# Optimization experiments

Measured on AMD Instinct MI355X. Metric: run time of the kernel, lower is better.

## Reference

```python
import jax, jax.numpy as jnp
import numpy as np

KSIZE, STRIDE, SCALE = 7, 4, 10.0


def _same_pad_amounts(n, k, s):
    out = -(-n // s)
    pad = max(0, (out - 1) * s + k - n)
    return pad // 2, pad - pad // 2, out


def _conv(x, w, b, stride=1, pad=0):
    y = jax.lax.conv_general_dilated(
        x, w, (stride, stride), [(pad, pad), (pad, pad)],
        dimension_numbers=("NCHW", "OIHW", "NCHW"))
    return y + b[None, :, None, None]


def setup_inputs() -> dict:
    key = jax.random.key(0)
    ks = jax.random.split(key, 10)
    B, Cin, H, W = 2, 64, 256, 256
    Ci = 16                       # inter_channels
    d_in = KSIZE * KSIZE * Ci     # 784 = ksize^2 * inter_channels
    d_out = d_in // 4             # 196
    s = 0.02
    return {
        "b": jax.random.normal(ks[0], (B, Cin, H, W), jnp.float32),
        "g_w": jax.random.normal(ks[1], (Ci, Cin, 3, 3), jnp.float32) * s,
        "g_b": jnp.zeros((Ci,), jnp.float32),
        "theta_w": jax.random.normal(ks[2], (Ci, Cin, 1, 1), jnp.float32) * s,
        "theta_b": jnp.zeros((Ci,), jnp.float32),
        "W_w": jax.random.normal(ks[3], (Cin, Ci, 1, 1), jnp.float32) * s,
        "W_b": jnp.zeros((Cin,), jnp.float32),
        "fc1_w": jax.random.normal(ks[4], (d_out, d_in), jnp.float32) * s,
        "fc1_b": jnp.zeros((d_out,), jnp.float32),
        "fc2_w": jax.random.normal(ks[5], (d_out, d_in), jnp.float32) * s,
        "fc2_b": jnp.zeros((d_out,), jnp.float32),
        "thr_w": jax.random.normal(ks[6], (1, Cin, KSIZE, KSIZE), jnp.float32) * s,
        "thr_b": jnp.zeros((1,), jnp.float32),
        "bias_w": jax.random.normal(ks[7], (1, Cin, KSIZE, KSIZE), jnp.float32) * s,
        "bias_b": jnp.zeros((1,), jnp.float32),
    }


def _forward(b, g_w, g_b, theta_w, theta_b, W_w, W_b, fc1_w, fc1_b,
             fc2_w, fc2_b, thr_w, thr_b, bias_w, bias_b):
    B, Cin, H, W = b.shape
    k, s = KSIZE, STRIDE
    pt, pb, Lh = _same_pad_amounts(H, k, s)
    pl, pr, Lw = _same_pad_amounts(W, k, s)
    L = Lh * Lw
    Ci = g_w.shape[0]

    b1 = _conv(b, g_w, g_b, 1, 1)            # [B,Ci,H,W]
    b2 = _conv(b, theta_w, theta_b, 1, 0)    # [B,Ci,H,W]
    b4 = jnp.pad(b, ((0, 0), (0, 0), (pt, pb), (pl, pr)))
    thr = _conv(b4, thr_w, thr_b, s, 0).reshape(B, L)   # per-patch threshold
    bias = _conv(b4, bias_w, bias_b, s, 0).reshape(B, L)  # per-patch bias

    # patch gather indices on the 'same'-padded grid (torch.Unfold order)
    R = (jnp.arange(Lh) * s)[:, None] + jnp.arange(k)[None, :]   # [Lh,k]
    Cc = (jnp.arange(Lw) * s)[:, None] + jnp.arange(k)[None, :]  # [Lw,k]
    Ri = R[:, None, :, None]                                     # -> [Lh,Lw,k,k]
    Cj = Cc[None, :, None, :]

    def patches(x):  # [B,Ci,H,W] -> [B,L,Ci*k*k], flatten order (C,kh,kw)
        xp = jnp.pad(x, ((0, 0), (0, 0), (pt, pb), (pl, pr)))
        p = xp[:, :, Ri, Cj]                       # [B,Ci,Lh,Lw,k,k]
        return p.transpose(0, 2, 3, 1, 4, 5).reshape(B, L, -1)

    wi = patches(b1)     # stride_1 patches of b1
    xi = wi              # b3 = b1 and stride_1 == stride_2 -> identical patches
    pi = patches(b2)     # stride_2 patches of b2, values to aggregate

    wi_f = jax.nn.relu(jnp.einsum("bld,od->blo", wi, fc1_w) + fc1_b)
    xi_f = jax.nn.relu(jnp.einsum("bld,od->blo", xi, fc2_w) + fc2_b)
    score = jnp.einsum("blo,bmo->blm", wi_f, xi_f)   # [B,L,L] patch similarity

    # threshold-gated sparse attention with learned per-patch thr/bias
    mask = (score >= thr[:, :, None]).astype(score.dtype)
    gated = score * mask + bias[:, :, None]
    attn = jax.nn.softmax(gated * SCALE, axis=-1) * mask
    attn = attn / (attn.sum(-1, keepdims=True) + 1e-8)

    agg = jnp.einsum("blm,bmd->bld", attn, pi)       # [B,L,Ci*k*k]
    p6 = agg.reshape(B, Lh, Lw, Ci, k, k).transpose(0, 3, 1, 2, 4, 5)

    # fold back (sum overlaps), normalize by overlap count, crop padding
    Hp, Wp = H + pt + pb, W + pl + pr
    folded = jnp.zeros((B, Ci, Hp, Wp), score.dtype).at[:, :, Ri, Cj].add(p6)
    cnt = jnp.zeros((Hp, Wp), score.dtype).at[Ri, Cj].add(1.0)
    zi = (folded / cnt)[:, :, pl:pl + H, pt:pt + W]

    return b + _conv(zi, W_w, W_b, 1, 0)


def reference(b, g_w, g_b, theta_w, theta_b, W_w, W_b, fc1_w, fc1_b,
              fc2_w, fc2_b, thr_w, thr_b, bias_w, bias_b):
    return _forward(b, g_w, g_b, theta_w, theta_b, W_w, W_b, fc1_w, fc1_b,
                    fc2_w, fc2_b, thr_w, thr_b, bias_w, bias_b)
```

## Files before the change

### kernel.cpp

```cpp
#include <hip/hip_runtime.h>
#include <math.h>

#define CIN  64
#define CI   16
#define HH   256
#define WWD  256
#define KS   7
#define STR  4
#define LH   64
#define LWD  64
#define LL   4096
#define DIN  784
#define DINP 896
#define DKP  832
#define DOUT 196
#define DOUTP 256
#define NB   2
#define YP   258
#define XP   264

typedef __attribute__((ext_vector_type(8))) short bf16x8;
typedef __attribute__((ext_vector_type(4))) float f32x4;
typedef __attribute__((ext_vector_type(16))) float f32x16;
typedef __attribute__((ext_vector_type(8))) int i32x8;
typedef __attribute__((ext_vector_type(4))) int i32x4;

__device__ __forceinline__ unsigned short f2bf(float x) {
    unsigned int u = __float_as_uint(x);
    unsigned int r = (u + 0x7FFFu + ((u >> 16) & 1u)) >> 16;
    return (unsigned short)r;
}
__device__ __forceinline__ float bf2f(unsigned short h) {
    return __uint_as_float(((unsigned int)h) << 16);
}

__device__ __forceinline__ void stage16(const void* g, void* l) {
#if defined(__has_builtin)
#if __has_builtin(__builtin_amdgcn_global_load_lds)
    __builtin_amdgcn_global_load_lds(
        (const __attribute__((address_space(1))) unsigned int*)g,
        (__attribute__((address_space(3))) unsigned int*)l, 16, 0, 0);
    return;
#endif
#endif
    *(float4*)l = *(const float4*)g;
}

__global__ __launch_bounds__(256) void k_prep_b(const float* __restrict__ b,
                                                unsigned short* __restrict__ bTp) {
    int blk = blockIdx.x;
    int s = blk & 7; int yy = (blk >> 3) % YP; int n = blk / (8 * YP);
    int y = yy - 1;
    for (int xx = threadIdx.x; xx < XP; xx += 256) {
        int x = xx - 4;
        bool v = (y >= 0 && y < 256 && x >= 0 && x < 256);
        unsigned short h[8];
#pragma unroll
        for (int j = 0; j < 8; j++)
            h[j] = v ? f2bf(b[((size_t)(n * 64 + s * 8 + j) * 256 + y) * 256 + x]) : (unsigned short)0;
        *(uint4*)&bTp[((((size_t)n * YP + yy) * 8 + s) * XP + xx) * 8] = *(uint4*)h;
    }
}

__global__ void k_prep_wb(const float* __restrict__ g_w, const float* __restrict__ th_w,
                          unsigned short* __restrict__ wbt) {
    int i = blockIdx.x * 256 + threadIdx.x;
    if (i >= 18432) return;
    int j = i & 7, co = (i >> 3) & 31, q = (i >> 8) & 3, h = (i >> 10) & 1, t = i >> 11;
    int ci = h * 32 + q * 8 + j;
    float v;
    if (co < 16) v = g_w[((size_t)co * 64 + ci) * 9 + t];
    else         v = (t == 4) ? th_w[(size_t)(co - 16) * 64 + ci] : 0.f;
    wbt[i] = f2bf(v);
}

__global__ void k_prep_fc(const float* __restrict__ fc1_w, const float* __restrict__ fc2_w,
                          unsigned short* __restrict__ fcwb) {
    int i = blockIdx.x * 256 + threadIdx.x;
    if (i >= 2 * DOUTP * DKP) return;
    int col = i % DKP; int row = (i / DKP) % DOUTP; int f = i / (DKP * DOUTP);
    float v = 0.f;
    if (row < DOUT && col < DIN) v = (f ? fc2_w : fc1_w)[row * DIN + col];
    fcwb[i] = f2bf(v);
}

__global__ __launch_bounds__(256) void k_convm(
        const unsigned short* __restrict__ bTp, const unsigned short* __restrict__ wbt,
        const float* __restrict__ g_b, const float* __restrict__ th_b,
        unsigned short* __restrict__ bx) {
    __shared__ unsigned short wb[18432];
    __shared__ unsigned short ti[8 * 3 * 68 * 8];
    int tid = threadIdx.x;
#pragma unroll
    for (int i = 0; i < 9; i++) {
        int c = i * 256 + tid;
        stage16(wbt + (size_t)c * 8, &wb[c * 8]);
    }
    int n = blockIdx.x >> 8, y = blockIdx.x & 255;
    int wave = tid >> 6, lane = tid & 63, lr = lane & 15, q = lane >> 4;
    int m0 = wave * 16;
    float bg = g_b[lr], bt = th_b[lr];
    for (int xs = 0; xs < 4; xs++) {
        __syncthreads();
        int x0 = xs * 64;
#pragma unroll
        for (int i = 0; i < 7; i++) {
            int c = i * 256 + tid;
            if (c < 1632) {
                int s = c / 204; int rem = c % 204; int r = rem / 68; int cc = rem % 68;
                const unsigned short* src =
                    bTp + ((((size_t)n * YP + y + r) * 8 + s) * XP + (x0 + 3 + cc)) * 8;
                stage16(src, &ti[c * 8]);
            }
        }
        __syncthreads();
        f32x4 a0 = {bg, bg, bg, bg}, a1 = {bt, bt, bt, bt};
#pragma unroll
        for (int t = 0; t < 9; t++) {
            int dy = t / 3, dx = t % 3;
#pragma unroll
            for (int h = 0; h < 2; h++) {
                int s = h * 4 + q;
                bf16x8 av = *(const bf16x8*)&ti[(((s * 3 + dy) * 68) + m0 + lr + dx) * 8];
                bf16x8 b0 = *(const bf16x8*)&wb[((((t * 2 + h) * 4 + q) * 32) + lr) * 8];
                bf16x8 b1 = *(const bf16x8*)&wb[((((t * 2 + h) * 4 + q) * 32) + 16 + lr) * 8];
                a0 = __builtin_amdgcn_mfma_f32_16x16x32_bf16(av, b0, a0, 0, 0, 0);
                a1 = __builtin_amdgcn_mfma_f32_16x16x32_bf16(av, b1, a1, 0, 0, 0);
            }
        }
        size_t pb = (((size_t)n * 256 + y) * 256 + x0 + m0 + q * 4);
#pragma unroll
        for (int r = 0; r < 4; r++) {
            bx[(pb + r) * 32 + lr]      = f2bf(a0[r]);
            bx[(pb + r) * 32 + 16 + lr] = f2bf(a1[r]);
        }
    }
}

__global__ __launch_bounds__(256) void k_thr(
        const unsigned short* __restrict__ bTp, const float* __restrict__ thr_w,
        const float* __restrict__ thr_b, float* __restrict__ thr) {
    __shared__ float w[64 * 49];
    int tid = threadIdx.x;
    for (int i = tid; i < 64 * 49; i += 256) w[i] = thr_w[i];
    __syncthreads();
    int wid = (blockIdx.x << 2) + (tid >> 6);
    int lane = tid & 63;
    int s = lane >> 3, j = lane & 7;
    int n = wid >> 12, l = wid & 4095;
    int lh = (l >> 6), lw = l & 63;
    const float* wl = w + (s * 8 + j) * 49;
    float acc = 0.f;
#pragma unroll
    for (int dy = 0; dy < 7; dy++) {
        int yy = lh * 4 + dy;
        if (yy >= YP) continue;
        const unsigned short* row = bTp + (((size_t)(n * YP + yy) * 8 + s) * XP) * 8;
#pragma unroll
        for (int dx = 0; dx < 7; dx++) {
            int xx = lw * 4 + dx + 3;
            acc = fmaf(bf2f(row[xx * 8 + j]), wl[dy * 7 + dx], acc);
        }
    }
#pragma unroll
    for (int off = 32; off > 0; off >>= 1) acc += __shfl_down(acc, off, 64);
    if (lane == 0) thr[wid] = acc + thr_b[0];
}

__global__ void k_patchesA(const unsigned short* __restrict__ bx, unsigned short* __restrict__ Pb) {
    size_t e = (size_t)blockIdx.x * 256 + threadIdx.x;
    if (e >= (size_t)NB * LL * DKP) return;
    int d = (int)(e % DKP); size_t r = e / DKP;
    int l = (int)(r & 4095); int n = (int)(r >> 12);
    unsigned short v = 0;
    if (d < DIN) {
        int ci = d / 49; int t = d % 49; int dy = t / 7; int dx = t % 7;
        int y = (l >> 6) * 4 + dy - 1, x = (l & 63) * 4 + dx - 1;
        if (y >= 0 && y < 256 && x >= 0 && x < 256)
            v = bx[(((size_t)n * 256 + y) * 256 + x) * 32 + ci];
    }
    Pb[e] = v;
}

__global__ void k_patchesT(const unsigned short* __restrict__ bx, unsigned char* __restrict__ piT8) {
    size_t e = (size_t)blockIdx.x * 256 + threadIdx.x;
    int l = (int)(e & 4095);
    int d = (int)((e >> 12) % DINP);
    int n = (int)(e / ((size_t)DINP * LL));
    float v = 0.f;
    if (d < DIN) {
        int ci = d / 49; int t = d % 49; int dy = t / 7; int dx = t % 7;
        int y = (l >> 6) * 4 + dy - 1, x = (l & 63) * 4 + dx - 1;
        if (y >= 0 && y < 256 && x >= 0 && x < 256)
            v = bf2f(bx[(((size_t)n * 256 + y) * 256 + x) * 32 + 16 + ci]);
    }
    int p = __builtin_amdgcn_cvt_pk_fp8_f32(v, 0.f, 0, false);
    piT8[e] = (unsigned char)(p & 0xFF);
}

template<int MODE>
__global__ __launch_bounds__(256) void k_gemm_nt(
        const unsigned short* __restrict__ A, const unsigned short* __restrict__ Bt,
        void* __restrict__ C, int lda, int ldb, int ldc, int K,
        size_t sA, size_t sB, size_t sC,
        const float* __restrict__ bias1, const float* __restrict__ bias2) {
    __shared__ unsigned short lA[128 * 64];
    __shared__ unsigned short lB[128 * 64];
    int tid = threadIdx.x;
    int wave = tid >> 6, lane = tid & 63;
    int lr = lane & 15, lq = lane >> 4;
    int wm = (wave >> 1) * 64, wn = (wave & 1) * 64;
    int i0 = blockIdx.x * 128, j0 = blockIdx.y * 128;
    int z = blockIdx.z;
    int az = (MODE == 2) ? (z >> 1) : z;
    int bz = (MODE == 2) ? (z & 1) : z;
    const unsigned short* Ab = A + (size_t)az * sA + (size_t)i0 * lda;
    const unsigned short* Bb = Bt + (size_t)bz * sB + (size_t)j0 * ldb;
    f32x4 acc[4][4] = {};
    for (int k0 = 0; k0 < K; k0 += 64) {
        __syncthreads();
#pragma unroll
        for (int it = 0; it < 4; it++) {
            int c = it * 256 + tid;
            int row = c >> 3, slot = c & 7;
            int col8 = slot ^ (row & 7);
            stage16(Ab + (size_t)row * lda + k0 + col8 * 8, &lA[c * 8]);
        }
#pragma unroll
        for (int it = 0; it < 4; it++) {
            int c = it * 256 + tid;
            int row = c >> 3, slot = c & 7;
            int col8 = slot ^ (row & 7);
            stage16(Bb + (size_t)row * ldb + k0 + col8 * 8, &lB[c * 8]);
        }
        __syncthreads();
#pragma unroll
        for (int ks = 0; ks < 2; ks++) {
            bf16x8 af[4], bfr[4];
#pragma unroll
            for (int t = 0; t < 4; t++) {
                int row = wm + t * 16 + lr;
                int slot = ks * 4 + lq;
                af[t] = *(const bf16x8*)&lA[row * 64 + (slot ^ (row & 7)) * 8];
            }
#pragma unroll
            for (int t = 0; t < 4; t++) {
                int row = wn + t * 16 + lr;
                int slot = ks * 4 + lq;
                bfr[t] = *(const bf16x8*)&lB[row * 64 + (slot ^ (row & 7)) * 8];
            }
#pragma unroll
            for (int mi = 0; mi < 4; mi++)
#pragma unroll
                for (int nj = 0; nj < 4; nj++)
                    acc[mi][nj] = __builtin_amdgcn_mfma_f32_16x16x32_bf16(
                        af[mi], bfr[nj], acc[mi][nj], 0, 0, 0);
        }
    }
    if (MODE == 1) {
        unsigned short* Cb = (unsigned short*)C + (size_t)z * sC;
#pragma unroll
        for (int mi = 0; mi < 4; mi++)
#pragma unroll
            for (int r = 0; r < 4; r++) {
                int row = i0 + wm + mi * 16 + lq * 4 + r;
#pragma unroll
                for (int nj = 0; nj < 4; nj++)
                    Cb[(size_t)row * ldc + j0 + wn + nj * 16 + lr] = f2bf(acc[mi][nj][r]);
            }
    } else {
        const float* biasp = bz ? bias2 : bias1;
        unsigned short* Cb = (unsigned short*)C + (size_t)z * sC;
#pragma unroll
        for (int mi = 0; mi < 4; mi++)
#pragma unroll
            for (int r = 0; r < 4; r++) {
                int row = i0 + wm + mi * 16 + lq * 4 + r;
#pragma unroll
                for (int nj = 0; nj < 4; nj++) {
                    int col = j0 + wn + nj * 16 + lr;
                    float bv = (col < DOUT) ? biasp[col] : 0.f;
                    float v = fmaxf(acc[mi][nj][r] + bv, 0.f);
                    Cb[(size_t)row * ldc + col] = f2bf(v);
                }
            }
    }
}

__global__ __launch_bounds__(256) void k_gemm_mx(
        const unsigned char* __restrict__ A, const unsigned char* __restrict__ Bt,
        unsigned short* __restrict__ C, int lda, int ldb, int ldc, int K,
        size_t sA, size_t sB, size_t sC) {
    __shared__ unsigned char lA[128 * 128];
    __shared__ unsigned char lB[128 * 128];
    int tid = threadIdx.x;
    int wave = tid >> 6, lane = tid & 63;
    int lr = lane & 31, hf = lane >> 5;
    int wm = (wave >> 1) * 64, wn = (wave & 1) * 64;
    int i0 = blockIdx.x * 128, j0 = blockIdx.y * 128;
    int z = blockIdx.z;
    const unsigned char* Ab = A + (size_t)z * sA + (size_t)i0 * lda;
    const unsigned char* Bb = Bt + (size_t)z * sB + (size_t)j0 * ldb;
    f32x16 acc[2][2] = {};
    for (int k0 = 0; k0 < K; k0 += 128) {
        __syncthreads();
#pragma unroll
        for (int it = 0; it < 4; it++) {
            int c = it * 256 + tid;
            int row = c >> 3, slot = c & 7;
            int col16 = slot ^ (row & 7);
            stage16(Ab + (size_t)row * lda + k0 + col16 * 16, &lA[c * 16]);
        }
#pragma unroll
        for (int it = 0; it < 4; it++) {
            int c = it * 256 + tid;
            int row = c >> 3, slot = c & 7;
            int col16 = slot ^ (row & 7);
            stage16(Bb + (size_t)row * ldb + k0 + col16 * 16, &lB[c * 16]);
        }
        __syncthreads();
#pragma unroll
        for (int kk = 0; kk < 2; kk++) {
            i32x8 af[2], bfv[2];
            int c0 = kk * 4 + hf * 2;
#pragma unroll
            for (int t = 0; t < 2; t++) {
                int row = wm + t * 32 + lr;
                i32x4 lo = *(const i32x4*)&lA[row * 128 + ((c0    ) ^ (row & 7)) * 16];
                i32x4 hi = *(const i32x4*)&lA[row * 128 + ((c0 + 1) ^ (row & 7)) * 16];
                af[t][0] = lo[0]; af[t][1] = lo[1]; af[t][2] = lo[2]; af[t][3] = lo[3];
                af[t][4] = hi[0]; af[t][5] = hi[1]; af[t][6] = hi[2]; af[t][7] = hi[3];
            }
#pragma unroll
            for (int t = 0; t < 2; t++) {
                int row = wn + t * 32 + lr;
                i32x4 lo = *(const i32x4*)&lB[row * 128 + ((c0    ) ^ (row & 7)) * 16];
                i32x4 hi = *(const i32x4*)&lB[row * 128 + ((c0 + 1) ^ (row & 7)) * 16];
                bfv[t][0] = lo[0]; bfv[t][1] = lo[1]; bfv[t][2] = lo[2]; bfv[t][3] = lo[3];
                bfv[t][4] = hi[0]; bfv[t][5] = hi[1]; bfv[t][6] = hi[2]; bfv[t][7] = hi[3];
            }
#pragma unroll
            for (int mi = 0; mi < 2; mi++)
#pragma unroll
                for (int nj = 0; nj < 2; nj++)
                    acc[mi][nj] = __builtin_amdgcn_mfma_scale_f32_32x32x64_f8f6f4(
                        af[mi], bfv[nj], acc[mi][nj],
                        0, 0,
                        0, 0x7F7F7F7F,
                        0, 0x7F7F7F7F);
        }
    }
    unsigned short* Cb = C + (size_t)z * sC;
#pragma unroll
    for (int mi = 0; mi < 2; mi++)
#pragma unroll
        for (int nj = 0; nj < 2; nj++)
#pragma unroll
            for (int reg = 0; reg < 16; reg++) {
                int row = i0 + wm + mi * 32 + (reg & 3) + 8 * (reg >> 2) + 4 * hf;
                int col = j0 + wn + nj * 32 + lr;
                Cb[(size_t)row * ldc + col] = f2bf(acc[mi][nj][reg]);
            }
}

__global__ __launch_bounds__(256) void k_softmax(
        const unsigned short* __restrict__ score, const float* __restrict__ thr,
        unsigned char* __restrict__ attn8) {
    __shared__ uint4 srow[512];
    __shared__ float red[256], red2[256];
    int row = blockIdx.x, tid = threadIdx.x;
    const uint4* g4 = (const uint4*)(score + (size_t)row * LL);
    float t = thr[row];
    float mx = 0.f;
#pragma unroll
    for (int c = tid; c < 512; c += 256) {
        uint4 u = g4[c];
        srow[c] = u;
        unsigned int w[4] = {u.x, u.y, u.z, u.w};
#pragma unroll
        for (int qq = 0; qq < 4; qq++) {
            float v0 = __uint_as_float(w[qq] << 16);
            float v1 = __uint_as_float(w[qq] & 0xFFFF0000u);
            if (v0 >= t) mx = fmaxf(mx, v0);
            if (v1 >= t) mx = fmaxf(mx, v1);
        }
    }
    red[tid] = mx; __syncthreads();
    for (int st = 128; st > 0; st >>= 1) {
        if (tid < st) red[tid] = fmaxf(red[tid], red[tid + st]);
        __syncthreads();
    }
    float M = 10.f * fmaxf(red[0], 0.f);
    __syncthreads();
    float s2 = 0.f, n0 = 0.f;
#pragma unroll
    for (int c = tid; c < 512; c += 256) {
        uint4 u = srow[c];
        unsigned int w[4] = {u.x, u.y, u.z, u.w};
#pragma unroll
        for (int qq = 0; qq < 4; qq++) {
            float v0 = __uint_as_float(w[qq] << 16);
            float v1 = __uint_as_float(w[qq] & 0xFFFF0000u);
            if (v0 >= t) s2 += __expf(10.f * v0 - M); else n0 += 1.f;
            if (v1 >= t) s2 += __expf(10.f * v1 - M); else n0 += 1.f;
        }
    }
    red[tid] = s2; red2[tid] = n0; __syncthreads();
    for (int st = 128; st > 0; st >>= 1) {
        if (tid < st) { red[tid] += red[tid + st]; red2[tid] += red2[tid + st]; }
        __syncthreads();
    }
    float S2 = red[0], N0 = red2[0];
    float iD = 1.f / (S2 + 1e-8f * (S2 + N0 * __expf(-M)));
#pragma unroll
    for (int c = tid; c < 512; c += 256) {
        uint4 u = srow[c];
        unsigned int w[4] = {u.x, u.y, u.z, u.w};
        float a[8];
#pragma unroll
        for (int qq = 0; qq < 4; qq++) {
            float v0 = __uint_as_float(w[qq] << 16);
            float v1 = __uint_as_float(w[qq] & 0xFFFF0000u);
            a[2 * qq]     = (v0 >= t) ? __expf(10.f * v0 - M) * iD : 0.f;
            a[2 * qq + 1] = (v1 >= t) ? __expf(10.f * v1 - M) * iD : 0.f;
        }
        int d0 = __builtin_amdgcn_cvt_pk_fp8_f32(a[0], a[1], 0, false);
        d0     = __builtin_amdgcn_cvt_pk_fp8_f32(a[2], a[3], d0, true);
        int d1 = __builtin_amdgcn_cvt_pk_fp8_f32(a[4], a[5], 0, false);
        d1     = __builtin_amdgcn_cvt_pk_fp8_f32(a[6], a[7], d1, true);
        *(uint2*)&attn8[(size_t)row * LL + c * 8] = make_uint2((unsigned)d0, (unsigned)d1);
    }
}

__global__ void k_fold(const unsigned short* __restrict__ aggb, float* __restrict__ zi) {
    int p = blockIdx.x * 256 + threadIdx.x;
    int x = p & 255, y = (p >> 8) & 255, ci = (p >> 16) & 15, n = p >> 20;
    int yp = y + 1, xp = x + 1;
    int lh1 = yp >> 2; if (lh1 > 63) lh1 = 63;
    int lh0 = (yp >= 3) ? ((yp - 3) >> 2) : 0;
    int lw1 = xp >> 2; if (lw1 > 63) lw1 = 63;
    int lw0 = (xp >= 3) ? ((xp - 3) >> 2) : 0;
    const unsigned short* a0 = aggb + (size_t)n * LL * DINP;
    float sum = 0.f;
    for (int lh = lh0; lh <= lh1; lh++) {
        int dy = yp - 4 * lh;
        for (int lw = lw0; lw <= lw1; lw++) {
            int dx = xp - 4 * lw;
            sum += bf2f(a0[(size_t)(lh * 64 + lw) * DINP + ci * 49 + dy * 7 + dx]);
        }
    }
    float cnt = (float)((lh1 - lh0 + 1) * (lw1 - lw0 + 1));
    zi[p] = sum / cnt;
}

__global__ void k_final(const float* __restrict__ zi, const float* __restrict__ b,
                        const float* __restrict__ W_w, const float* __restrict__ W_b,
                        float* __restrict__ out) {
    __shared__ float w[16 * 64];
    int tid = threadIdx.x;
    for (int i = tid; i < 16 * 64; i += 256) {
        int ci = i >> 6; int co = i & 63;
        w[i] = W_w[co * 16 + ci];
    }
    __syncthreads();
    int p = blockIdx.x * 256 + tid;
    int n = p >> 16, yx = p & 65535;
    float acc[64];
#pragma unroll
    for (int co = 0; co < 64; co++) acc[co] = 0.f;
    const float* zn = zi + (size_t)n * 16 * 65536;
#pragma unroll
    for (int ci = 0; ci < 16; ci++) {
        float v = zn[ci * 65536 + yx];
#pragma unroll
        for (int co = 0; co < 64; co++) acc[co] += v * w[ci * 64 + co];
    }
    const float* bn = b + (size_t)n * 64 * 65536;
    float* on = out + (size_t)n * 64 * 65536;
#pragma unroll
    for (int co = 0; co < 64; co++) on[co * 65536 + yx] = bn[co * 65536 + yx] + acc[co] + W_b[co];
}

extern "C" void kernel_launch(void* const* d_in, const int* in_sizes, int n_in,
                              void* d_out, int out_size, void* d_ws, size_t ws_size,
                              hipStream_t stream) {
    const float* b     = (const float*)d_in[0];
    const float* g_w   = (const float*)d_in[1];
    const float* g_b   = (const float*)d_in[2];
    const float* th_w  = (const float*)d_in[3];
    const float* th_b  = (const float*)d_in[4];
    const float* W_w   = (const float*)d_in[5];
    const float* W_b   = (const float*)d_in[6];
    const float* fc1_w = (const float*)d_in[7];
    const float* fc1_b = (const float*)d_in[8];
    const float* fc2_w = (const float*)d_in[9];
    const float* fc2_b = (const float*)d_in[10];
    const float* thr_w = (const float*)d_in[11];
    const float* thr_b = (const float*)d_in[12];
    float* out = (float*)d_out;

    float* ws = (float*)d_ws;
    size_t off = 0;
    auto alloc = [&](size_t nf) { float* p = ws + off; off += (nf + 63) & ~(size_t)63; return p; };
    unsigned short* aggb = (unsigned short*)alloc((size_t)NB * LL * DINP / 2);
    float* zi   = alloc((size_t)NB * CI * HH * WWD);
    unsigned short* bTp  = (unsigned short*)alloc((size_t)NB * YP * 8 * XP * 8 / 2);
    unsigned short* bx   = (unsigned short*)alloc((size_t)NB * HH * WWD * 32 / 2);
    unsigned short* Pb   = (unsigned short*)alloc((size_t)NB * LL * DKP / 2);
    unsigned char*  piT8 = (unsigned char*)alloc((size_t)NB * DINP * LL / 4);
    unsigned short* fcout = (unsigned short*)alloc((size_t)NB * 2 * LL * DOUTP / 2);
    unsigned short* wbt  = (unsigned short*)alloc(18432 / 2);
    unsigned short* fcwb = (unsigned short*)alloc((size_t)2 * DOUTP * DKP / 2);
    float* thr  = alloc((size_t)NB * LL);
    unsigned short* score = (unsigned short*)alloc((size_t)NB * LL * LL / 2);
    unsigned char*  attn8 = (unsigned char*)alloc((size_t)NB * LL * LL / 4);

    k_prep_b<<<dim3(NB * YP * 8), 256, 0, stream>>>(b, bTp);
    k_prep_wb<<<dim3(72), 256, 0, stream>>>(g_w, th_w, wbt);
    k_prep_fc<<<dim3((2 * DOUTP * DKP + 255) / 256), 256, 0, stream>>>(fc1_w, fc2_w, fcwb);
    k_convm<<<dim3(NB * 256), 256, 0, stream>>>(bTp, wbt, g_b, th_b, bx);
    k_thr<<<dim3(2048), 256, 0, stream>>>(bTp, thr_w, thr_b, thr);
    k_patchesA<<<dim3((int)((size_t)NB * LL * DKP / 256)), 256, 0, stream>>>(bx, Pb);
    k_patchesT<<<dim3((int)((size_t)NB * DINP * LL / 256)), 256, 0, stream>>>(bx, piT8);
    k_gemm_nt<2><<<dim3(32, 2, 4), 256, 0, stream>>>(
        Pb, fcwb, (void*)fcout, DKP, DKP, DOUTP, DKP,
        (size_t)LL * DKP, (size_t)DOUTP * DKP, (size_t)LL * DOUTP, fc1_b, fc2_b);
    k_gemm_nt<1><<<dim3(32, 32, NB), 256, 0, stream>>>(
        fcout, fcout + (size_t)LL * DOUTP, (void*)score, DOUTP, DOUTP, LL, DOUTP,
        (size_t)2 * LL * DOUTP, (size_t)2 * LL * DOUTP, (size_t)LL * LL, nullptr, nullptr);
    k_softmax<<<dim3(NB * LL), 256, 0, stream>>>(score, thr, attn8);
    k_gemm_mx<<<dim3(32, DINP / 128, NB), 256, 0, stream>>>(
        attn8, piT8, aggb, LL, LL, DINP, LL,
        (size_t)LL * LL, (size_t)DINP * LL, (size_t)LL * DINP);
    k_fold<<<dim3(8192), 256, 0, stream>>>(aggb, zi);
    k_final<<<dim3(512), 256, 0, stream>>>(zi, b, W_w, W_b, out);
}
```

Before: 330.8 us.

## Fuse fold into final conv and cache softmax exponentials in shared memory

```diff
diff --git a/kernel.cpp b/kernel.cpp
--- a/kernel.cpp
+++ b/kernel.cpp
@@ -345,9 +345,7 @@
                 for (int nj = 0; nj < 2; nj++)
                     acc[mi][nj] = __builtin_amdgcn_mfma_scale_f32_32x32x64_f8f6f4(
                         af[mi], bfv[nj], acc[mi][nj],
-                        0, 0,
-                        0, 0x7F7F7F7F,
-                        0, 0x7F7F7F7F);
+                        0, 0, 0, 0x7F7F7F7F, 0, 0x7F7F7F7F);
         }
     }
     unsigned short* Cb = C + (size_t)z * sC;
@@ -367,6 +365,7 @@
         const unsigned short* __restrict__ score, const float* __restrict__ thr,
         unsigned char* __restrict__ attn8) {
     __shared__ uint4 srow[512];
+    __shared__ float se[4096];
     __shared__ float red[256], red2[256];
     int row = blockIdx.x, tid = threadIdx.x;
     const uint4* g4 = (const uint4*)(score + (size_t)row * LL);
@@ -401,8 +400,11 @@
         for (int qq = 0; qq < 4; qq++) {
             float v0 = __uint_as_float(w[qq] << 16);
             float v1 = __uint_as_float(w[qq] & 0xFFFF0000u);
-            if (v0 >= t) s2 += __expf(10.f * v0 - M); else n0 += 1.f;
-            if (v1 >= t) s2 += __expf(10.f * v1 - M); else n0 += 1.f;
+            float e0 = 0.f, e1 = 0.f;
+            if (v0 >= t) { e0 = __expf(10.f * v0 - M); s2 += e0; } else n0 += 1.f;
+            if (v1 >= t) { e1 = __expf(10.f * v1 - M); s2 += e1; } else n0 += 1.f;
+            se[((2 * qq)     << 9) | c] = e0;
+            se[((2 * qq + 1) << 9) | c] = e1;
         }
     }
     red[tid] = s2; red2[tid] = n0; __syncthreads();
@@ -414,16 +416,9 @@
     float iD = 1.f / (S2 + 1e-8f * (S2 + N0 * __expf(-M)));
 #pragma unroll
     for (int c = tid; c < 512; c += 256) {
-        uint4 u = srow[c];
-        unsigned int w[4] = {u.x, u.y, u.z, u.w};
         float a[8];
 #pragma unroll
-        for (int qq = 0; qq < 4; qq++) {
-            float v0 = __uint_as_float(w[qq] << 16);
-            float v1 = __uint_as_float(w[qq] & 0xFFFF0000u);
-            a[2 * qq]     = (v0 >= t) ? __expf(10.f * v0 - M) * iD : 0.f;
-            a[2 * qq + 1] = (v1 >= t) ? __expf(10.f * v1 - M) * iD : 0.f;
-        }
+        for (int i = 0; i < 8; i++) a[i] = se[(i << 9) | c] * iD;
         int d0 = __builtin_amdgcn_cvt_pk_fp8_f32(a[0], a[1], 0, false);
         d0     = __builtin_amdgcn_cvt_pk_fp8_f32(a[2], a[3], d0, true);
         int d1 = __builtin_amdgcn_cvt_pk_fp8_f32(a[4], a[5], 0, false);
@@ -432,53 +427,50 @@
     }
 }
 
-__global__ void k_fold(const unsigned short* __restrict__ aggb, float* __restrict__ zi) {
+__global__ __launch_bounds__(256) void k_foldfinal(
+        const unsigned short* __restrict__ aggb, const unsigned short* __restrict__ bTp,
+        const float* __restrict__ W_w, const float* __restrict__ W_b,
+        float* __restrict__ out) {
     int p = blockIdx.x * 256 + threadIdx.x;
-    int x = p & 255, y = (p >> 8) & 255, ci = (p >> 16) & 15, n = p >> 20;
+    int x = p & 255, y = (p >> 8) & 255, n = p >> 16;
     int yp = y + 1, xp = x + 1;
     int lh1 = yp >> 2; if (lh1 > 63) lh1 = 63;
     int lh0 = (yp >= 3) ? ((yp - 3) >> 2) : 0;
     int lw1 = xp >> 2; if (lw1 > 63) lw1 = 63;
     int lw0 = (xp >= 3) ? ((xp - 3) >> 2) : 0;
     const unsigned short* a0 = aggb + (size_t)n * LL * DINP;
-    float sum = 0.f;
+    float icnt = 1.f / (float)((lh1 - lh0 + 1) * (lw1 - lw0 + 1));
+    float zloc[16];
+#pragma unroll
+    for (int ci = 0; ci < 16; ci++) zloc[ci] = 0.f;
     for (int lh = lh0; lh <= lh1; lh++) {
         int dy = yp - 4 * lh;
         for (int lw = lw0; lw <= lw1; lw++) {
             int dx = xp - 4 * lw;
-            sum += bf2f(a0[(size_t)(lh * 64 + lw) * DINP + ci * 49 + dy * 7 + dx]);
-        }
-    }
-    float cnt = (float)((lh1 - lh0 + 1) * (lw1 - lw0 + 1));
-    zi[p] = sum / cnt;
-}
-
-__global__ void k_final(const float* __restrict__ zi, const float* __restrict__ b,
-                        const float* __restrict__ W_w, const float* __restrict__ W_b,
-                        float* __restrict__ out) {
-    __shared__ float w[16 * 64];
-    int tid = threadIdx.x;
-    for (int i = tid; i < 16 * 64; i += 256) {
-        int ci = i >> 6; int co = i & 63;
-        w[i] = W_w[co * 16 + ci];
-    }
-    __syncthreads();
-    int p = blockIdx.x * 256 + tid;
-    int n = p >> 16, yx = p & 65535;
-    float acc[64];
-#pragma unroll
-    for (int co = 0; co < 64; co++) acc[co] = 0.f;
-    const float* zn = zi + (size_t)n * 16 * 65536;
-#pragma unroll
-    for (int ci = 0; ci < 16; ci++) {
-        float v = zn[ci * 65536 + yx];
-#pragma unroll
-        for (int co = 0; co < 64; co++) acc[co] += v * w[ci * 64 + co];
-    }
-    const float* bn = b + (size_t)n * 64 * 65536;
-    float* on = out + (size_t)n * 64 * 65536;
-#pragma unroll
-    for (int co = 0; co < 64; co++) on[co * 65536 + yx] = bn[co * 65536 + yx] + acc[co] + W_b[co];
+            const unsigned short* ap = a0 + (size_t)(lh * 64 + lw) * DINP + dy * 7 + dx;
+#pragma unroll
+            for (int ci = 0; ci < 16; ci++) zloc[ci] += bf2f(ap[ci * 49]);
+        }
+    }
+#pragma unroll
+    for (int ci = 0; ci < 16; ci++) zloc[ci] *= icnt;
+    float* on = out + (size_t)n * 64 * 65536 + (y * 256 + x);
+#pragma unroll
+    for (int s = 0; s < 8; s++) {
+        uint4 b8 = *(const uint4*)&bTp[((((size_t)n * YP + y + 1) * 8 + s) * XP + x + 4) * 8];
+        unsigned int bw[4] = {b8.x, b8.y, b8.z, b8.w};
+#pragma unroll
+        for (int j = 0; j < 8; j++) {
+            int co = s * 8 + j;
+            float acc = W_b[co];
+#pragma unroll
+            for (int ci = 0; ci < 16; ci++)
+                acc = fmaf(zloc[ci], W_w[co * 16 + ci], acc);
+            unsigned int hw = bw[j >> 1];
+            float bres = __uint_as_float((j & 1) ? (hw & 0xFFFF0000u) : (hw << 16));
+            on[(size_t)co * 65536] = bres + acc;
+        }
+    }
 }
 
 extern "C" void kernel_launch(void* const* d_in, const int* in_sizes, int n_in,
@@ -503,7 +495,6 @@
     size_t off = 0;
     auto alloc = [&](size_t nf) { float* p = ws + off; off += (nf + 63) & ~(size_t)63; return p; };
     unsigned short* aggb = (unsigned short*)alloc((size_t)NB * LL * DINP / 2);
-    float* zi   = alloc((size_t)NB * CI * HH * WWD);
     unsigned short* bTp  = (unsigned short*)alloc((size_t)NB * YP * 8 * XP * 8 / 2);
     unsigned short* bx   = (unsigned short*)alloc((size_t)NB * HH * WWD * 32 / 2);
     unsigned short* Pb   = (unsigned short*)alloc((size_t)NB * LL * DKP / 2);
@@ -532,6 +523,5 @@
     k_gemm_mx<<<dim3(32, DINP / 128, NB), 256, 0, stream>>>(
         attn8, piT8, aggb, LL, LL, DINP, LL,
         (size_t)LL * LL, (size_t)DINP * LL, (size_t)LL * DINP);
-    k_fold<<<dim3(8192), 256, 0, stream>>>(aggb, zi);
-    k_final<<<dim3(512), 256, 0, stream>>>(zi, b, W_w, W_b, out);
-}
+    k_foldfinal<<<dim3(512), 256, 0, stream>>>(aggb, bTp, W_w, W_b, out);
+}
```

Measured after the change: 331.7 us. About the same (+0.3%).
